# Kernel optimization log

Hardware: AMD Instinct MI355X
Metric: run time of the kernel (lower is better)

## Reference

```python
import jax, jax.numpy as jnp
import numpy as np

N_NODES = 50000
N_EDGES = 500000
D_MODEL = 128
EDGE_DIM = 16
LN_EPS = 1e-5


def setup_inputs() -> dict:
    key = jax.random.key(0)
    ks = jax.random.split(key, 12)
    s = 0.05
    return {
        "x_src": jax.random.normal(ks[0], (N_NODES, D_MODEL), jnp.float32),
        "x_dst": jax.random.normal(ks[1], (N_NODES, D_MODEL), jnp.float32),
        "edge_src": jax.random.randint(ks[2], (N_EDGES,), 0, N_NODES, jnp.int32),
        "edge_dst": jax.random.randint(ks[3], (N_EDGES,), 0, N_NODES, jnp.int32),
        "edge_attr": jax.random.normal(ks[4], (N_EDGES, EDGE_DIM), jnp.float32),
        "W_src": jax.random.normal(ks[5], (D_MODEL, D_MODEL), jnp.float32) * s,
        "W_dst": jax.random.normal(ks[6], (D_MODEL, D_MODEL), jnp.float32) * s,
        "b_dst": jnp.zeros((D_MODEL,), jnp.float32),
        "gate_w1": jax.random.normal(ks[7], (D_MODEL, EDGE_DIM), jnp.float32) * s,
        "gate_b1": jnp.zeros((D_MODEL,), jnp.float32),
        "gate_w2": jax.random.normal(ks[8], (1, D_MODEL), jnp.float32) * s,
        "gate_b2": jnp.zeros((1,), jnp.float32),
        "ln_gamma": jnp.ones((D_MODEL,), jnp.float32),
        "ln_beta": jnp.zeros((D_MODEL,), jnp.float32),
    }


def _layernorm(x, gamma, beta):
    mu = jnp.mean(x, axis=-1, keepdims=True)
    var = jnp.mean(jnp.square(x - mu), axis=-1, keepdims=True)
    return (x - mu) * jax.lax.rsqrt(var + LN_EPS) * gamma + beta


def reference(x_src, x_dst, edge_src, edge_dst, edge_attr,
              W_src, W_dst, b_dst, gate_w1, gate_b1, gate_w2, gate_b2,
              ln_gamma, ln_beta):
    n_dst = x_dst.shape[0]
    # gather + linear message: [E, d]
    msg = jnp.einsum('ed,fd->ef', x_src[edge_src], W_src)
    # edge-gate MLP (norm=False, eval mode -> no dropout): Linear -> gelu -> Linear -> sigmoid
    g = jax.nn.gelu(edge_attr @ gate_w1.T + gate_b1, approximate=False)
    gate = jax.nn.sigmoid(g @ gate_w2.T + gate_b2)  # [E, 1]
    msg = msg * gate
    # scatter-add aggregation and degree normalization
    agg = jax.ops.segment_sum(msg, edge_dst, num_segments=n_dst)
    deg = jax.ops.segment_sum(jnp.ones((edge_dst.shape[0],), msg.dtype), edge_dst,
                              num_segments=n_dst)
    agg = agg / jnp.maximum(deg, 1.0)[:, None]
    out = _layernorm(agg + x_dst @ W_dst.T + b_dst, ln_gamma, ln_beta)
    return jax.nn.gelu(out, approximate=False)
```

## Files before the change

kernel.cpp:

```cpp
#include <hip/hip_runtime.h>

#define D_MODEL 128
#define EDGE_DIM 16

typedef __attribute__((ext_vector_type(8))) short bf16x8;
typedef __attribute__((ext_vector_type(4))) float f32x4;

__device__ __forceinline__ float sigmoid_fast(float a) {
    return 1.0f / (1.0f + __expf(-a));
}
__device__ __forceinline__ float gelu_tanh(float x) {
    float x2  = x * x;
    float arg = x * fmaf(0.07135481627f, x2, 1.59576912161f);
    return x * sigmoid_fast(arg);
}

__device__ __forceinline__ float gelu_poly(float x) {
    float s = fminf(x * x, 2.89f);
    float r = fmaf(-9.4447e-6f, s, 1.154347e-4f);
    r = fmaf(r, s, -1.1873282e-3f);
    r = fmaf(r, s, 9.9735570e-3f);
    r = fmaf(r, s, -6.64903801e-2f);
    r = fmaf(r, s, 3.989422804e-1f);
    return fmaf(s, r, 0.5f * x);
}

__device__ __forceinline__ unsigned short f2bf(float x) {
    unsigned u = __float_as_uint(x);
    u += 0x7FFFu + ((u >> 16) & 1u);
    return (unsigned short)(u >> 16);
}

__global__ __launch_bounds__(256) void wt_kernel(
    const float* __restrict__ Wsrc, const float* __restrict__ Wdst,
    unsigned short* __restrict__ wTfrag)
{
    int i = blockIdx.x * 256 + threadIdx.x;
    if (i >= 8 * 8 * 64) return;
    int kc = i >> 9;
    int ft = (i >> 6) & 7;
    int l  = i & 63;
    int f  = ft * 16 + (l & 15);
    int d0 = kc * 32 + (l >> 4) * 8;
    const float* src = (d0 < D_MODEL) ? (Wsrc + (size_t)f * D_MODEL + d0)
                                      : (Wdst + (size_t)f * D_MODEL + (d0 - D_MODEL));
    unsigned short* dst = wTfrag + (size_t)i * 8;
#pragma unroll
    for (int v = 0; v < 8; v++) dst[v] = f2bf(src[v]);
}

__global__ __launch_bounds__(256) void hist_kernel(
    const int* __restrict__ edst, int* __restrict__ degi, int E)
{
    int e = blockIdx.x * 256 + threadIdx.x;
    if (e < E) atomicAdd(&degi[edst[e]], 1);
}

__global__ __launch_bounds__(256) void scan1_kernel(
    const int* __restrict__ degi, int* __restrict__ starts,
    int* __restrict__ partials, int N)
{
    __shared__ int sm[256];
    int t = threadIdx.x;
    int idx = blockIdx.x * 256 + t;
    int val = (idx < N) ? degi[idx] : 0;
    sm[t] = val;
    __syncthreads();
#pragma unroll
    for (int off = 1; off < 256; off <<= 1) {
        int x = (t >= off) ? sm[t - off] : 0;
        __syncthreads();
        sm[t] += x;
        __syncthreads();
    }
    if (idx < N) starts[idx] = sm[t] - val;
    if (t == 255) partials[blockIdx.x] = sm[255];
}

__global__ __launch_bounds__(256) void scan2_kernel(
    int* __restrict__ partials, int nblocks)
{
    __shared__ int sm[256];
    int t = threadIdx.x;
    int val = (t < nblocks) ? partials[t] : 0;
    sm[t] = val;
    __syncthreads();
#pragma unroll
    for (int off = 1; off < 256; off <<= 1) {
        int x = (t >= off) ? sm[t - off] : 0;
        __syncthreads();
        sm[t] += x;
        __syncthreads();
    }
    if (t < nblocks) partials[t] = sm[t] - val;
}

__global__ __launch_bounds__(256) void scan3_kernel(
    int* __restrict__ starts, int* __restrict__ cursor,
    const int* __restrict__ partials, int N)
{
    int idx = blockIdx.x * 256 + threadIdx.x;
    if (idx < N) {
        int s = starts[idx] + partials[idx >> 8];
        starts[idx] = s;
        cursor[idx] = s;
    }
}

__global__ __launch_bounds__(256) void gate_scatter_kernel(
    const float* __restrict__ eattr,
    const float* __restrict__ gw1, const float* __restrict__ gb1,
    const float* __restrict__ gw2, const float* __restrict__ gb2,
    const int* __restrict__ esrc, const int* __restrict__ edst,
    int* __restrict__ cursor,
    int* __restrict__ sorted_src, float* __restrict__ sorted_gate, int E)
{
    int lane = threadIdx.x & 63;
    int wid  = threadIdx.x >> 6;
    int col  = lane & 15;
    int half = lane >> 4;

    bf16x8 bfrag[8];
    float  w2v[8], b1v[8];
#pragma unroll
    for (int jt = 0; jt < 8; jt++) {
        int j = jt * 16 + col;
        w2v[jt] = gw2[j];
        b1v[jt] = gb1[j];
        bf16x8 bf = {0, 0, 0, 0, 0, 0, 0, 0};
        if (half < 2) {
            const float4* wp = (const float4*)(gw1 + j * EDGE_DIM + half * 8);
            float4 u0 = wp[0], u1 = wp[1];
            bf[0] = (short)f2bf(u0.x); bf[1] = (short)f2bf(u0.y);
            bf[2] = (short)f2bf(u0.z); bf[3] = (short)f2bf(u0.w);
            bf[4] = (short)f2bf(u1.x); bf[5] = (short)f2bf(u1.y);
            bf[6] = (short)f2bf(u1.z); bf[7] = (short)f2bf(u1.w);
        }
        bfrag[jt] = bf;
    }
    float b2v = gb2[0];

    int ebase = blockIdx.x * 256 + wid * 64;
    for (int g = 0; g < 4; g++) {
        int e0 = ebase + g * 16;
        if (e0 >= E) break;

        int e = e0 + col;
        bf16x8 afrag = {0, 0, 0, 0, 0, 0, 0, 0};
        if (half < 2 && e < E) {
            const float4* ap = (const float4*)(eattr + (size_t)e * EDGE_DIM + half * 8);
            float4 a0 = ap[0], a1 = ap[1];
            afrag[0] = (short)f2bf(a0.x); afrag[1] = (short)f2bf(a0.y);
            afrag[2] = (short)f2bf(a0.z); afrag[3] = (short)f2bf(a0.w);
            afrag[4] = (short)f2bf(a1.x); afrag[5] = (short)f2bf(a1.y);
            afrag[6] = (short)f2bf(a1.z); afrag[7] = (short)f2bf(a1.w);
        }

        float p0 = 0.f, p1 = 0.f, p2 = 0.f, p3 = 0.f;
#pragma unroll
        for (int jt = 0; jt < 8; jt++) {
            f32x4 c = {0.f, 0.f, 0.f, 0.f};
            c = __builtin_amdgcn_mfma_f32_16x16x32_bf16(afrag, bfrag[jt], c, 0, 0, 0);
            p0 = fmaf(gelu_poly(c[0] + b1v[jt]), w2v[jt], p0);
            p1 = fmaf(gelu_poly(c[1] + b1v[jt]), w2v[jt], p1);
            p2 = fmaf(gelu_poly(c[2] + b1v[jt]), w2v[jt], p2);
            p3 = fmaf(gelu_poly(c[3] + b1v[jt]), w2v[jt], p3);
        }
#pragma unroll
        for (int m = 8; m >= 1; m >>= 1) {
            p0 += __shfl_xor(p0, m, 64);
            p1 += __shfl_xor(p1, m, 64);
            p2 += __shfl_xor(p2, m, 64);
            p3 += __shfl_xor(p3, m, 64);
        }
        if (col < 4) {
            float logit = (col == 0) ? p0 : (col == 1) ? p1 : (col == 2) ? p2 : p3;
            int er = e0 + half * 4 + col;
            if (er < E) {
                float gt = sigmoid_fast(logit + b2v);
                int dv = edst[er];
                int sv = esrc[er];
                int pos = atomicAdd(&cursor[dv], 1);
                sorted_src[pos]  = sv;
                sorted_gate[pos] = gt;
            }
        }
    }
}

__global__ __launch_bounds__(256) void agg_kernel(
    const float* __restrict__ x_src,
    const int* __restrict__ sorted_src, const float* __restrict__ sorted_gate,
    const int* __restrict__ starts, const int* __restrict__ degi,
    float* __restrict__ h, int N)
{
    int gid  = blockIdx.x * 256 + threadIdx.x;
    int wave = gid >> 6;
    int lane = gid & 63;
    int half = lane >> 5;
    int li   = lane & 31;
    int n    = wave * 2 + half;
    if (n >= N) return;

    int begin = starts[n];
    int cnt   = degi[n];

    float4 accv = make_float4(0.f, 0.f, 0.f, 0.f);
    int i = 0;
    for (; i + 2 <= cnt; i += 2) {
        int   sA = sorted_src[begin + i];
        int   sB = sorted_src[begin + i + 1];
        float gA = sorted_gate[begin + i];
        float gB = sorted_gate[begin + i + 1];
        float4 vA = ((const float4*)(x_src + (size_t)sA * D_MODEL))[li];
        float4 vB = ((const float4*)(x_src + (size_t)sB * D_MODEL))[li];
        accv.x += gA * vA.x + gB * vB.x;
        accv.y += gA * vA.y + gB * vB.y;
        accv.z += gA * vA.z + gB * vB.z;
        accv.w += gA * vA.w + gB * vB.w;
    }
    if (i < cnt) {
        int   s = sorted_src[begin + i];
        float g = sorted_gate[begin + i];
        float4 v = ((const float4*)(x_src + (size_t)s * D_MODEL))[li];
        accv.x += g * v.x;
        accv.y += g * v.y;
        accv.z += g * v.z;
        accv.w += g * v.w;
    }
    float r = 1.0f / (float)max(cnt, 1);
    accv.x *= r; accv.y *= r; accv.z *= r; accv.w *= r;
    *(float4*)(h + (size_t)n * D_MODEL + li * 4) = accv;
}

#define NT 64

__global__ __launch_bounds__(256) void node_kernel(
    const float* __restrict__ h,
    const float* __restrict__ x_dst, const unsigned short* __restrict__ wTfrag,
    const float* __restrict__ bdst, const float* __restrict__ gamma_,
    const float* __restrict__ beta_, float* __restrict__ out, int N)
{
    int lane = threadIdx.x & 63;
    int wid  = threadIdx.x >> 6;
    int col  = lane & 15;
    int half = lane >> 4;
    int base = blockIdx.x * NT + wid * 16;
    if (base >= N) return;

    int arow = base + col;
    bool aok = arow < N;
    const float* hrow = h     + (size_t)arow * D_MODEL + half * 8;
    const float* xrow = x_dst + (size_t)arow * D_MODEL + half * 8;

    f32x4 acc[8];
#pragma unroll
    for (int ft = 0; ft < 8; ft++) acc[ft] = (f32x4){0.f, 0.f, 0.f, 0.f};

    const bf16x8* bbase = ((const bf16x8*)wTfrag) + lane;

#pragma unroll
    for (int kc = 0; kc < 8; kc++) {
        bf16x8 afrag = {0, 0, 0, 0, 0, 0, 0, 0};
        if (aok) {
            const float* ap = (kc < 4) ? (hrow + kc * 32) : (xrow + (kc - 4) * 32);
            float4 a0 = ((const float4*)ap)[0];
            float4 a1 = ((const float4*)ap)[1];
            afrag[0] = (short)f2bf(a0.x); afrag[1] = (short)f2bf(a0.y);
            afrag[2] = (short)f2bf(a0.z); afrag[3] = (short)f2bf(a0.w);
            afrag[4] = (short)f2bf(a1.x); afrag[5] = (short)f2bf(a1.y);
            afrag[6] = (short)f2bf(a1.z); afrag[7] = (short)f2bf(a1.w);
        }
        const bf16x8* bk = bbase + (size_t)kc * 512;
#pragma unroll
        for (int ft = 0; ft < 8; ft++) {
            bf16x8 bfrag = bk[ft * 64];
            acc[ft] = __builtin_amdgcn_mfma_f32_16x16x32_bf16(afrag, bfrag, acc[ft], 0, 0, 0);
        }
    }

    float bv[8], gv[8], ev[8];
#pragma unroll
    for (int ft = 0; ft < 8; ft++) {
        int f = ft * 16 + col;
        bv[ft] = bdst[f];
        gv[ft] = gamma_[f];
        ev[ft] = beta_[f];
    }

#pragma unroll
    for (int r = 0; r < 4; r++) {
        int nr = base + half * 4 + r;
        float yv[8];
        float s1 = 0.f, s2 = 0.f;
#pragma unroll
        for (int ft = 0; ft < 8; ft++) {
            float x = acc[ft][r] + bv[ft];
            yv[ft] = x;
            s1 += x;
            s2 += x * x;
        }
#pragma unroll
        for (int m = 8; m >= 1; m >>= 1) {
            s1 += __shfl_xor(s1, m, 64);
            s2 += __shfl_xor(s2, m, 64);
        }
        float mu   = s1 * (1.0f / 128.0f);
        float var  = s2 * (1.0f / 128.0f) - mu * mu;
        float rstd = rsqrtf(var + 1e-5f);
        if (nr < N) {
            float* op = out + (size_t)nr * D_MODEL + col;
#pragma unroll
            for (int ft = 0; ft < 8; ft++)
                op[ft * 16] = gelu_tanh((yv[ft] - mu) * rstd * gv[ft] + ev[ft]);
        }
    }
}

extern "C" void kernel_launch(void* const* d_in, const int* in_sizes, int n_in,
                              void* d_out, int out_size, void* d_ws, size_t ws_size,
                              hipStream_t stream) {
    const float* x_src  = (const float*)d_in[0];
    const float* x_dst  = (const float*)d_in[1];
    const int*   esrc   = (const int*)d_in[2];
    const int*   edst   = (const int*)d_in[3];
    const float* eattr  = (const float*)d_in[4];
    const float* Wsrc   = (const float*)d_in[5];
    const float* Wdst   = (const float*)d_in[6];
    const float* bdst   = (const float*)d_in[7];
    const float* gw1    = (const float*)d_in[8];
    const float* gb1    = (const float*)d_in[9];
    const float* gw2    = (const float*)d_in[10];
    const float* gb2    = (const float*)d_in[11];
    const float* gamma_ = (const float*)d_in[12];
    const float* beta_  = (const float*)d_in[13];
    float* out = (float*)d_out;

    int E = in_sizes[2];
    int N = in_sizes[1] / D_MODEL;

    char* ws = (char*)d_ws;
    size_t off = 0;
    auto alloc = [&](size_t bytes) {
        size_t cur = off;
        off = (off + bytes + 255) & ~(size_t)255;
        return (void*)(ws + cur);
    };
    unsigned short* wTfrag = (unsigned short*)alloc((size_t)8 * 8 * 64 * 8 * 2);
    int*   degi        = (int*)  alloc((size_t)N * 4);
    int*   starts      = (int*)  alloc((size_t)N * 4);
    int*   cursor      = (int*)  alloc((size_t)N * 4);
    int*   partials    = (int*)  alloc(256 * 4);
    int*   sorted_src  = (int*)  alloc((size_t)E * 4);
    float* sorted_gate = (float*)alloc((size_t)E * 4);
    float* h           = (float*)alloc((size_t)N * D_MODEL * 4);

    int nblocksN = (N + 255) / 256;
    int nblocksE = (E + 255) / 256;
    int nblocksG = (E + 255) / 256;

    hipMemsetAsync(degi, 0, (size_t)N * 4, stream);

    wt_kernel<<<16, 256, 0, stream>>>(Wsrc, Wdst, wTfrag);
    hist_kernel<<<nblocksE, 256, 0, stream>>>(edst, degi, E);
    scan1_kernel<<<nblocksN, 256, 0, stream>>>(degi, starts, partials, N);
    scan2_kernel<<<1, 256, 0, stream>>>(partials, nblocksN);
    scan3_kernel<<<nblocksN, 256, 0, stream>>>(starts, cursor, partials, N);
    gate_scatter_kernel<<<nblocksG, 256, 0, stream>>>(
        eattr, gw1, gb1, gw2, gb2, esrc, edst, cursor, sorted_src, sorted_gate, E);
    agg_kernel<<<((size_t)N * 32 + 255) / 256, 256, 0, stream>>>(
        x_src, sorted_src, sorted_gate, starts, degi, h, N);
    node_kernel<<<(N + NT - 1) / NT, 256, 0, stream>>>(
        h, x_dst, wTfrag, bdst, gamma_, beta_, out, N);
}
```

Baseline: 260.9 us.

## Split gate MLP from counting-sort scatter into separate kernels

The fused gate+scatter kernel is split in two. A gate_kernel computes the edge gates with MFMA, then uses lane shuffles to lay the results out so each lane writes one gate in a coalesced store to an intermediate buffer. A simple per-edge scatter_kernel then does the atomic cursor placement with full-lane utilization, where before only 8 lanes of each 16-edge group did atomics. This adds one extra kernel launch and an extra E-float write and read.

```diff
diff --git a/kernel.cpp b/kernel.cpp
--- a/kernel.cpp
+++ b/kernel.cpp
@@ -107,13 +107,11 @@
     }
 }
 
-__global__ __launch_bounds__(256) void gate_scatter_kernel(
+__global__ __launch_bounds__(256) void gate_kernel(
     const float* __restrict__ eattr,
     const float* __restrict__ gw1, const float* __restrict__ gb1,
     const float* __restrict__ gw2, const float* __restrict__ gb2,
-    const int* __restrict__ esrc, const int* __restrict__ edst,
-    int* __restrict__ cursor,
-    int* __restrict__ sorted_src, float* __restrict__ sorted_gate, int E)
+    float* __restrict__ gate_out, int E)
 {
     int lane = threadIdx.x & 63;
     int wid  = threadIdx.x >> 6;
@@ -141,51 +139,70 @@
     float b2v = gb2[0];
 
     int ebase = blockIdx.x * 256 + wid * 64;
+    float q[4] = {0.f, 0.f, 0.f, 0.f};
+
+#pragma unroll
     for (int g = 0; g < 4; g++) {
         int e0 = ebase + g * 16;
-        if (e0 >= E) break;
-
-        int e = e0 + col;
-        bf16x8 afrag = {0, 0, 0, 0, 0, 0, 0, 0};
-        if (half < 2 && e < E) {
-            const float4* ap = (const float4*)(eattr + (size_t)e * EDGE_DIM + half * 8);
-            float4 a0 = ap[0], a1 = ap[1];
-            afrag[0] = (short)f2bf(a0.x); afrag[1] = (short)f2bf(a0.y);
-            afrag[2] = (short)f2bf(a0.z); afrag[3] = (short)f2bf(a0.w);
-            afrag[4] = (short)f2bf(a1.x); afrag[5] = (short)f2bf(a1.y);
-            afrag[6] = (short)f2bf(a1.z); afrag[7] = (short)f2bf(a1.w);
-        }
-
-        float p0 = 0.f, p1 = 0.f, p2 = 0.f, p3 = 0.f;
-#pragma unroll
-        for (int jt = 0; jt < 8; jt++) {
-            f32x4 c = {0.f, 0.f, 0.f, 0.f};
-            c = __builtin_amdgcn_mfma_f32_16x16x32_bf16(afrag, bfrag[jt], c, 0, 0, 0);
-            p0 = fmaf(gelu_poly(c[0] + b1v[jt]), w2v[jt], p0);
-            p1 = fmaf(gelu_poly(c[1] + b1v[jt]), w2v[jt], p1);
-            p2 = fmaf(gelu_poly(c[2] + b1v[jt]), w2v[jt], p2);
-            p3 = fmaf(gelu_poly(c[3] + b1v[jt]), w2v[jt], p3);
-        }
-#pragma unroll
-        for (int m = 8; m >= 1; m >>= 1) {
-            p0 += __shfl_xor(p0, m, 64);
-            p1 += __shfl_xor(p1, m, 64);
-            p2 += __shfl_xor(p2, m, 64);
-            p3 += __shfl_xor(p3, m, 64);
-        }
-        if (col < 4) {
-            float logit = (col == 0) ? p0 : (col == 1) ? p1 : (col == 2) ? p2 : p3;
-            int er = e0 + half * 4 + col;
-            if (er < E) {
-                float gt = sigmoid_fast(logit + b2v);
-                int dv = edst[er];
-                int sv = esrc[er];
-                int pos = atomicAdd(&cursor[dv], 1);
-                sorted_src[pos]  = sv;
-                sorted_gate[pos] = gt;
+        if (e0 < E) {
+            int e = e0 + col;
+            bf16x8 afrag = {0, 0, 0, 0, 0, 0, 0, 0};
+            if (half < 2 && e < E) {
+                const float4* ap = (const float4*)(eattr + (size_t)e * EDGE_DIM + half * 8);
+                float4 a0 = ap[0], a1 = ap[1];
+                afrag[0] = (short)f2bf(a0.x); afrag[1] = (short)f2bf(a0.y);
+                afrag[2] = (short)f2bf(a0.z); afrag[3] = (short)f2bf(a0.w);
+                afrag[4] = (short)f2bf(a1.x); afrag[5] = (short)f2bf(a1.y);
+                afrag[6] = (short)f2bf(a1.z); afrag[7] = (short)f2bf(a1.w);
             }
-        }
-    }
+
+            float p0 = 0.f, p1 = 0.f, p2 = 0.f, p3 = 0.f;
+#pragma unroll
+            for (int jt = 0; jt < 8; jt++) {
+                f32x4 c = {0.f, 0.f, 0.f, 0.f};
+                c = __builtin_amdgcn_mfma_f32_16x16x32_bf16(afrag, bfrag[jt], c, 0, 0, 0);
+                p0 = fmaf(gelu_poly(c[0] + b1v[jt]), w2v[jt], p0);
+                p1 = fmaf(gelu_poly(c[1] + b1v[jt]), w2v[jt], p1);
+                p2 = fmaf(gelu_poly(c[2] + b1v[jt]), w2v[jt], p2);
+                p3 = fmaf(gelu_poly(c[3] + b1v[jt]), w2v[jt], p3);
+            }
+#pragma unroll
+            for (int m = 8; m >= 1; m >>= 1) {
+                p0 += __shfl_xor(p0, m, 64);
+                p1 += __shfl_xor(p1, m, 64);
+                p2 += __shfl_xor(p2, m, 64);
+                p3 += __shfl_xor(p3, m, 64);
+            }
+            int r3 = lane & 3;
+            q[g] = (r3 == 0) ? p0 : (r3 == 1) ? p1 : (r3 == 2) ? p2 : p3;
+        }
+    }
+
+    int src = ((lane & 15) >> 2) * 16 + (lane & 3);
+    float t0 = __shfl(q[0], src, 64);
+    float t1 = __shfl(q[1], src, 64);
+    float t2 = __shfl(q[2], src, 64);
+    float t3 = __shfl(q[3], src, 64);
+    int gsel = lane >> 4;
+    float logit = (gsel == 0) ? t0 : (gsel == 1) ? t1 : (gsel == 2) ? t2 : t3;
+    int e = ebase + lane;
+    if (e < E) gate_out[e] = sigmoid_fast(logit + b2v);
+}
+
+__global__ __launch_bounds__(256) void scatter_kernel(
+    const float* __restrict__ gate_out,
+    const int* __restrict__ esrc, const int* __restrict__ edst,
+    int* __restrict__ cursor,
+    int* __restrict__ sorted_src, float* __restrict__ sorted_gate, int E)
+{
+    int e = blockIdx.x * 256 + threadIdx.x;
+    if (e >= E) return;
+    float g = gate_out[e];
+    int  dv = edst[e];
+    int  sv = esrc[e];
+    int pos = atomicAdd(&cursor[dv], 1);
+    sorted_src[pos]  = sv;
+    sorted_gate[pos] = g;
 }
 
 __global__ __launch_bounds__(256) void agg_kernel(
@@ -353,21 +370,23 @@
     int*   partials    = (int*)  alloc(256 * 4);
     int*   sorted_src  = (int*)  alloc((size_t)E * 4);
     float* sorted_gate = (float*)alloc((size_t)E * 4);
+    float* gate_out    = (float*)alloc((size_t)E * 4);
     float* h           = (float*)alloc((size_t)N * D_MODEL * 4);
 
     int nblocksN = (N + 255) / 256;
     int nblocksE = (E + 255) / 256;
-    int nblocksG = (E + 255) / 256;
 
     hipMemsetAsync(degi, 0, (size_t)N * 4, stream);
 
     wt_kernel<<<16, 256, 0, stream>>>(Wsrc, Wdst, wTfrag);
+    gate_kernel<<<nblocksE, 256, 0, stream>>>(
+        eattr, gw1, gb1, gw2, gb2, gate_out, E);
     hist_kernel<<<nblocksE, 256, 0, stream>>>(edst, degi, E);
     scan1_kernel<<<nblocksN, 256, 0, stream>>>(degi, starts, partials, N);
     scan2_kernel<<<1, 256, 0, stream>>>(partials, nblocksN);
     scan3_kernel<<<nblocksN, 256, 0, stream>>>(starts, cursor, partials, N);
-    gate_scatter_kernel<<<nblocksG, 256, 0, stream>>>(
-        eattr, gw1, gb1, gw2, gb2, esrc, edst, cursor, sorted_src, sorted_gate, E);
+    scatter_kernel<<<nblocksE, 256, 0, stream>>>(
+        gate_out, esrc, edst, cursor, sorted_src, sorted_gate, E);
     agg_kernel<<<((size_t)N * 32 + 255) / 256, 256, 0, stream>>>(
         x_src, sorted_src, sorted_gate, starts, degi, h, N);
     node_kernel<<<(N + NT - 1) / NT, 256, 0, stream>>>(
```

Result: slower. 271.9 us (+4.2%).
